# Kernel tuning notes

Hardware: AMD Instinct MI355X
Metric: run time of the kernel (lower is better)

Reference implementation:

```python
import jax, jax.numpy as jnp
import numpy as np

V, D_IMG, D_H = 10000, 768, 512
B, N, T = 16, 196, 128
LN_EPS = 1e-5

def _lin_w(k, fan_out, fan_in):
    bound = 1.0 / np.sqrt(fan_in)
    return jax.random.uniform(k, (fan_out, fan_in), jnp.float32, -bound, bound)

def _lin_b(k, fan_out, fan_in):
    bound = 1.0 / np.sqrt(fan_in)
    return jax.random.uniform(k, (fan_out,), jnp.float32, -bound, bound)

def setup_inputs() -> dict:
    key = jax.random.key(0)
    ks = jax.random.split(key, 24)
    patches = jax.random.normal(ks[0], (B, N, D_IMG), jnp.float32)
    cls = jax.random.normal(ks[1], (B, D_IMG), jnp.float32)
    tgt_ids = jax.random.randint(ks[2], (B, T), 0, V)
    emb = jax.random.normal(ks[3], (V, D_H), jnp.float32)
    emb = emb.at[0].set(0.0)  # padding_idx=0
    inp = {
        "patches": patches, "cls": cls, "tgt_ids": tgt_ids,
        "kv_w": _lin_w(ks[4], D_H, D_IMG), "kv_b": _lin_b(ks[5], D_H, D_IMG),
        "ih_w": _lin_w(ks[6], D_H, D_IMG), "ih_b": _lin_b(ks[7], D_H, D_IMG),
        "ic_w": _lin_w(ks[8], D_H, D_IMG), "ic_b": _lin_b(ks[9], D_H, D_IMG),
        "emb": emb,
        "attn_Wh": _lin_w(ks[10], D_H, D_H),
        "attn_Wk": _lin_w(ks[11], D_H, D_H),
        "attn_v": _lin_w(ks[12], 1, D_H),
        "lstm_Wih": _lin_w(ks[13], 4 * D_H, D_H),  # pytorch init uses 1/sqrt(hidden)
        "lstm_Whh": _lin_w(ks[14], 4 * D_H, D_H),
        "lstm_bih": _lin_b(ks[15], 4 * D_H, D_H),
        "lstm_bhh": _lin_b(ks[16], 4 * D_H, D_H),
        "ln_g": jnp.ones((D_H,), jnp.float32),
        "ln_b": jnp.zeros((D_H,), jnp.float32),
        "out_w": _lin_w(ks[17], V, D_H), "out_b": _lin_b(ks[18], V, D_H),
    }
    # lstm_Wih actually has fan_in 2*D_H but torch inits with 1/sqrt(hidden_size); reshape to correct shape
    inp["lstm_Wih"] = _lin_w(ks[19], 4 * D_H, 2 * D_H)
    return inp

def _layernorm(x, g, b):
    mu = jnp.mean(x, -1, keepdims=True)
    var = jnp.mean(jnp.square(x - mu), -1, keepdims=True)
    return (x - mu) * jax.lax.rsqrt(var + LN_EPS) * g + b

def reference(patches, cls, tgt_ids, kv_w, kv_b, ih_w, ih_b, ic_w, ic_b, emb,
              attn_Wh, attn_Wk, attn_v, lstm_Wih, lstm_Whh, lstm_bih, lstm_bhh,
              ln_g, ln_b, out_w, out_b):
    keys = patches @ kv_w.T + kv_b            # (B,N,d_h)
    keysWk = keys @ attn_Wk.T                 # precompute W_k(keys), loop-invariant
    h0 = cls @ ih_w.T + ih_b                  # (B,d_h)
    c0 = cls @ ic_w.T + ic_b
    x_all = emb[tgt_ids]                      # (B,T,d_h)
    vvec = attn_v[0]                          # (d_h,)

    def step(carry, x_t):
        h, c = carry
        energy = jnp.tanh((h @ attn_Wh.T)[:, None, :] + keysWk)   # (B,N,d_h)
        scores = energy @ vvec                                    # (B,N)
        alpha = jax.nn.softmax(scores, axis=-1)
        ctx = jnp.einsum('bn,bnd->bd', alpha, keys)               # (B,d_h)
        z = jnp.concatenate([x_t, ctx], axis=-1)                  # (B,2*d_h)
        gates = z @ lstm_Wih.T + lstm_bih + h @ lstm_Whh.T + lstm_bhh
        i, f, g, o = jnp.split(gates, 4, axis=-1)
        c_new = jax.nn.sigmoid(f) * c + jax.nn.sigmoid(i) * jnp.tanh(g)
        h_raw = jax.nn.sigmoid(o) * jnp.tanh(c_new)
        h_new = _layernorm(h_raw, ln_g, ln_b)  # dropout is identity in eval
        logits_t = h_new @ out_w.T + out_b     # (B,V)
        return (h_new, c_new), logits_t

    (_, _), logits = jax.lax.scan(step, (h0, c0), jnp.swapaxes(x_all, 0, 1))
    return jnp.swapaxes(logits, 0, 1)          # (B,T,V)
```

## Files before the change

### kernel.cpp

```cpp
#include <hip/hip_runtime.h>
#include <hip/hip_bf16.h>

#define T_STEPS 128
#define DH      512
#define NPATCH  196
#define BATCH   16
#define VOCAB   10000
#define NB5     64

typedef __attribute__((ext_vector_type(8))) short bf16x8;
typedef __attribute__((ext_vector_type(4))) float f32x4;

__device__ __forceinline__ float sigm(float x) { return 1.0f / (1.0f + __expf(-x)); }
__device__ __forceinline__ float ftanh(float x) {
    float e = __expf(2.0f * x);
    return 1.0f - 2.0f / (e + 1.0f);
}
__device__ __forceinline__ unsigned short f2b(float x) {
    union { float f; unsigned u; } v; v.f = x;
    unsigned r = (v.u + 0x7FFFu + ((v.u >> 16) & 1u)) >> 16;
    return (unsigned short)r;
}
__device__ __forceinline__ float b2f(unsigned short h) {
    union { unsigned u; float f; } v; v.u = ((unsigned)h) << 16;
    return v.f;
}
__device__ __forceinline__ float cload(const float* p) {
    return __hip_atomic_load(p, __ATOMIC_RELAXED, __HIP_MEMORY_SCOPE_AGENT);
}
__device__ __forceinline__ void cstore(float* p, float v) {
    __hip_atomic_store(p, v, __ATOMIC_RELAXED, __HIP_MEMORY_SCOPE_AGENT);
}
__device__ __forceinline__ f32x4 cload4(const float* p) {
    f32x4 v;
    asm volatile("global_load_dwordx4 %0, %1, off sc0 sc1\n\ts_waitcnt vmcnt(0)"
                 : "=&v"(v) : "v"(p) : "memory");
    return v;
}
__device__ __forceinline__ void cload4x2(const float* p0, const float* p1, f32x4& a, f32x4& b) {
    asm volatile("global_load_dwordx4 %0, %2, off sc0 sc1\n\t"
                 "global_load_dwordx4 %1, %3, off sc0 sc1\n\t"
                 "s_waitcnt vmcnt(0)"
                 : "=&v"(a), "=&v"(b) : "v"(p0), "v"(p1) : "memory");
}
__device__ __forceinline__ void cstore4(float* p, f32x4 v) {
    asm volatile("global_store_dwordx4 %0, %1, off sc0 sc1" :: "v"(p), "v"(v) : "memory");
}

__global__ __launch_bounds__(256)
void cvt_kernel(const float* __restrict__ src, unsigned short* __restrict__ dst, int n)
{
    int i = (blockIdx.x * 256 + threadIdx.x) * 8;
    if (i >= n) return;
    float4 v0 = *(const float4*)(src + i);
    float4 v1 = *(const float4*)(src + i + 4);
    float xs[8] = {v0.x, v0.y, v0.z, v0.w, v1.x, v1.y, v1.z, v1.w};
    bf16x8 o;
#pragma unroll
    for (int j = 0; j < 8; ++j) o[j] = (short)f2b(xs[j]);
    *(bf16x8*)(dst + i) = o;
}

__global__ __launch_bounds__(256)
void cvt_split_kernel(const float* __restrict__ src, unsigned short* __restrict__ hi,
                      unsigned short* __restrict__ lo, int n)
{
    int i = (blockIdx.x * 256 + threadIdx.x) * 8;
    if (i >= n) return;
    float4 v0 = *(const float4*)(src + i);
    float4 v1 = *(const float4*)(src + i + 4);
    float xs[8] = {v0.x, v0.y, v0.z, v0.w, v1.x, v1.y, v1.z, v1.w};
    bf16x8 h_, l_;
#pragma unroll
    for (int j = 0; j < 8; ++j) {
        unsigned short hb = f2b(xs[j]);
        float r = xs[j] - b2f(hb);
        h_[j] = (short)hb;
        l_[j] = (short)f2b(r);
    }
    *(bf16x8*)(hi + i) = h_;
    *(bf16x8*)(lo + i) = l_;
}

__global__ __launch_bounds__(256)
void cvt_wx_kernel(const float* __restrict__ Wih, unsigned short* __restrict__ WxH,
                   unsigned short* __restrict__ WxL)
{
    int i = (blockIdx.x * 256 + threadIdx.x) * 8;
    if (i >= 2048 * 512) return;
    int j = i >> 9, k = i & 511;
    const float* s = Wih + (size_t)j * 1024 + k;
    float4 v0 = *(const float4*)s, v1 = *(const float4*)(s + 4);
    float xs[8] = {v0.x, v0.y, v0.z, v0.w, v1.x, v1.y, v1.z, v1.w};
    bf16x8 h_, l_;
#pragma unroll
    for (int q = 0; q < 8; ++q) {
        unsigned short hb = f2b(xs[q]);
        h_[q] = (short)hb;
        l_[q] = (short)f2b(xs[q] - b2f(hb));
    }
    *(bf16x8*)(WxH + i) = h_;
    *(bf16x8*)(WxL + i) = l_;
}

__global__ __launch_bounds__(256)
void gemm_mfma(const unsigned short* __restrict__ AH, const unsigned short* __restrict__ AL,
               const unsigned short* __restrict__ WH, const unsigned short* __restrict__ WL,
               const float* __restrict__ bias, float* __restrict__ C,
               unsigned short* __restrict__ CbH, unsigned short* __restrict__ CbL,
               int M, int N, int K)
{
    const int tid = threadIdx.x, wid = tid >> 6, l = tid & 63;
    const int m0 = blockIdx.x * 128 + (wid >> 1) * 64;
    const int n0 = blockIdx.y * 128 + (wid & 1) * 64;
    const int lm = l & 15, lk = (l >> 4) * 8;
    f32x4 acc[4][4];
#pragma unroll
    for (int i = 0; i < 4; ++i)
#pragma unroll
        for (int j = 0; j < 4; ++j) acc[i][j] = (f32x4){0.f, 0.f, 0.f, 0.f};
    const bf16x8 az = {0,0,0,0,0,0,0,0};

    for (int k0 = 0; k0 < K; k0 += 32) {
        bf16x8 aH[4], aL[4];
#pragma unroll
        for (int mi = 0; mi < 4; ++mi) {
            int m = m0 + mi * 16 + lm;
            aH[mi] = (m < M) ? *(const bf16x8*)(AH + (size_t)m * K + k0 + lk) : az;
            aL[mi] = (AL && m < M) ? *(const bf16x8*)(AL + (size_t)m * K + k0 + lk) : az;
        }
#pragma unroll
        for (int ni = 0; ni < 4; ++ni) {
            int n = n0 + ni * 16 + lm;
            bf16x8 bH = az, bL = az;
            if (n < N) {
                bH = *(const bf16x8*)(WH + (size_t)n * K + k0 + lk);
                if (WL) bL = *(const bf16x8*)(WL + (size_t)n * K + k0 + lk);
            }
#pragma unroll
            for (int mi = 0; mi < 4; ++mi) {
                acc[mi][ni] = __builtin_amdgcn_mfma_f32_16x16x32_bf16(aH[mi], bH, acc[mi][ni], 0, 0, 0);
                if (WL) acc[mi][ni] = __builtin_amdgcn_mfma_f32_16x16x32_bf16(aH[mi], bL, acc[mi][ni], 0, 0, 0);
                if (AL) acc[mi][ni] = __builtin_amdgcn_mfma_f32_16x16x32_bf16(aL[mi], bH, acc[mi][ni], 0, 0, 0);
            }
        }
    }
    const int rr = (l >> 4) * 4;
#pragma unroll
    for (int mi = 0; mi < 4; ++mi) {
        int mb = m0 + mi * 16 + rr;
#pragma unroll
        for (int ni = 0; ni < 4; ++ni) {
            int n = n0 + ni * 16 + lm;
            if (n < N) {
                float bs = bias ? bias[n] : 0.f;
#pragma unroll
                for (int r = 0; r < 4; ++r) {
                    int mm = mb + r;
                    if (mm < M) {
                        float v = acc[mi][ni][r] + bs;
                        if (C)   C[(size_t)mm * N + n] = v;
                        if (CbH) {
                            unsigned short hb = f2b(v);
                            CbH[(size_t)mm * N + n] = hb;
                            if (CbL) CbL[(size_t)mm * N + n] = f2b(v - b2f(hb));
                        }
                    }
                }
            }
        }
    }
}

__global__ __launch_bounds__(256)
void h0c0_kernel(const float* __restrict__ cls,
                 const float* __restrict__ ihw, const float* __restrict__ ihb,
                 const float* __restrict__ icw, const float* __restrict__ icb,
                 float* __restrict__ c_g, float* __restrict__ h_raw0)
{
    int id = blockIdx.x * 256 + threadIdx.x;
    int which = id >> 13;
    int b = (id >> 9) & 15;
    int d = id & 511;
    const float* w = (which ? icw : ihw) + d * 768;
    const float* x = cls + b * 768;
    float acc = which ? icb[d] : ihb[d];
    const float4* x4 = (const float4*)x;
    const float4* w4 = (const float4*)w;
#pragma unroll 4
    for (int k = 0; k < 192; ++k) {
        float4 a = x4[k], ww = w4[k];
        acc += a.x * ww.x + a.y * ww.y + a.z * ww.z + a.w * ww.w;
    }
    if (which) c_g[b * 512 + d] = acc;
    else h_raw0[b * 512 + d] = acc;
}

__global__ __launch_bounds__(256)
void gather_kernel(const int* __restrict__ ids, const float* __restrict__ emb,
                   unsigned short* __restrict__ xH, unsigned short* __restrict__ xL)
{
    int q = blockIdx.x * 256 + threadIdx.x;
    if (q >= 2048 * 64) return;
    int r = q >> 6, c = (q & 63) * 8;
    int tgt = ids[r];
    const float4* s = (const float4*)(emb + (size_t)tgt * 512 + c);
    float4 v0 = s[0], v1 = s[1];
    float xs[8] = {v0.x, v0.y, v0.z, v0.w, v1.x, v1.y, v1.z, v1.w};
    bf16x8 oh, ol;
#pragma unroll
    for (int j = 0; j < 8; ++j) {
        unsigned short hb = f2b(xs[j]);
        oh[j] = (short)hb;
        ol[j] = (short)f2b(xs[j] - b2f(hb));
    }
    *(bf16x8*)(xH + (size_t)r * 512 + c) = oh;
    *(bf16x8*)(xL + (size_t)r * 512 + c) = ol;
}

__device__ __forceinline__ void grid_bar(int* slots, int gen)
{
    __syncthreads();
    if (threadIdx.x < 64) {
        if (threadIdx.x == 0)
            __hip_atomic_store(&slots[blockIdx.x], gen, __ATOMIC_RELAXED, __HIP_MEMORY_SCOPE_AGENT);
        while (__hip_atomic_load(&slots[threadIdx.x], __ATOMIC_RELAXED, __HIP_MEMORY_SCOPE_AGENT) < gen)
            __builtin_amdgcn_s_sleep(1);
    }
    __syncthreads();
}
__device__ __forceinline__ void group_bar(int* gslots, int b_own, int q, int gen)
{
    __syncthreads();
    if (threadIdx.x < 4) {
        if (threadIdx.x == 0)
            __hip_atomic_store(&gslots[b_own * 4 + q], gen, __ATOMIC_RELAXED, __HIP_MEMORY_SCOPE_AGENT);
        while (__hip_atomic_load(&gslots[b_own * 4 + threadIdx.x], __ATOMIC_RELAXED, __HIP_MEMORY_SCOPE_AGENT) < gen)
            __builtin_amdgcn_s_sleep(1);
    }
    __syncthreads();
}

__global__ __launch_bounds__(1024, 2)
void recur6_kernel(float* __restrict__ ctx, float* __restrict__ hln_g,
                   float* __restrict__ h_raw2, float* __restrict__ c_g,
                   float* __restrict__ partials2, float* __restrict__ ew_g,
                   float* __restrict__ sc_g,
                   const float* __restrict__ keys, const float* __restrict__ keysWk,
                   const float* __restrict__ XG,
                   const float* __restrict__ Wih, const float* __restrict__ Whh,
                   const float* __restrict__ bih, const float* __restrict__ bhh,
                   const float* __restrict__ Wh, const float* __restrict__ lng,
                   const float* __restrict__ lnb, const float* __restrict__ vvec,
                   unsigned short* __restrict__ h_all_b, int* __restrict__ bar)
{
    __shared__ float zs[8][1024];
    __shared__ float hv[512], ewS[512], vvS[512];
    __shared__ float alS[200];
    __shared__ float pb[8][128];
    __shared__ float gbuf[16][32];
    __shared__ float bias_l[32], red[32];

    const int k = blockIdx.x, tid = threadIdx.x;
    const int b_own = k & 15, q = k >> 4;
    const int rrow = tid >> 5, ks = tid & 31;
    int* gslots = bar + 64;

    float wreg[32];
    {
        int g = rrow >> 3, dd = rrow & 7;
        int j = g * 512 + 8 * k + dd;
        const float* wc = Wih + (size_t)j * 1024 + 512;
        const float* wh2 = Whh + (size_t)j * 512;
#pragma unroll
        for (int i = 0; i < 32; ++i) {
            int kk = ks + 32 * i;
            wreg[i] = (kk < 512) ? wc[kk] : wh2[kk - 512];
        }
        if (tid < 32) {
            int g2 = tid >> 3, dd2 = tid & 7, j2 = g2 * 512 + 8 * k + dd2;
            bias_l[tid] = bih[j2] + bhh[j2];
        }
        if (tid < 512) vvS[tid] = vvec[tid];
    }
    __syncthreads();

    int gen = 0;
    for (int t = 0; t < T_STEPS; ++t) {
        const float* hcur = h_raw2 + (t & 1) * (BATCH * 512);
        float* hnxt = h_raw2 + ((t + 1) & 1) * (BATCH * 512);
        const float* pcur = partials2 + (t & 1) * (BATCH * 64 * 2);
        float* pnxt = partials2 + ((t + 1) & 1) * (BATCH * 64 * 2);

        if (t > 0) {
            if (tid < 64) {
                const float* pp = pcur + ((size_t)b_own * 64 + tid) * 2;
                float s1 = cload(pp), s2 = cload(pp + 1);
#pragma unroll
                for (int m = 1; m < 64; m <<= 1) { s1 += __shfl_xor(s1, m); s2 += __shfl_xor(s2, m); }
                if (tid == 0) {
                    float mu = s1 * (1.f / 512.f);
                    float var = s2 * (1.f / 512.f) - mu * mu;
                    red[0] = mu; red[1] = rsqrtf(var + 1e-5f);
                }
            }
        } else if (tid == 0) { red[0] = 0.f; red[1] = 1.f; }
        __syncthreads();
        if (tid < 128) {
            f32x4 h4 = cload4(hcur + b_own * 512 + tid * 4);
            f32x4 o = h4;
            if (t > 0) {
                float mu = red[0], rv = red[1];
                f32x4 g4 = ((const f32x4*)lng)[tid];
                f32x4 bl4 = ((const f32x4*)lnb)[tid];
#pragma unroll
                for (int u = 0; u < 4; ++u) o[u] = (h4[u] - mu) * rv * g4[u] + bl4[u];
            }
            ((f32x4*)hv)[tid] = o;
            if (q == 0) {
                cstore4(&hln_g[b_own * 512 + tid * 4], o);
                if (t > 0) {
                    short4 hb = { (short)f2b(o[0]), (short)f2b(o[1]), (short)f2b(o[2]), (short)f2b(o[3]) };
                    *(short4*)(h_all_b + ((size_t)b_own * T_STEPS + (t - 1)) * 512 + tid * 4) = hb;
                }
            }
        }
        __syncthreads();
        {
            int e = q * 128 + (tid >> 3), g8 = tid & 7;
            const float4* wr4 = (const float4*)(Wh + (size_t)e * 512);
            float s = 0.f;
#pragma unroll
            for (int i = 0; i < 16; ++i) {
                int k4 = g8 + 8 * i;
                float4 w4 = wr4[k4];
                float4 h4 = ((const float4*)hv)[k4];
                s += w4.x * h4.x + w4.y * h4.y + w4.z * h4.z + w4.w * h4.w;
            }
            s += __shfl_xor(s, 1); s += __shfl_xor(s, 2); s += __shfl_xor(s, 4);
            if (g8 == 0) cstore(&ew_g[b_own * 512 + e], s);
        }
        group_bar(gslots, b_own, q, ++gen);

        if (tid < 128) ((f32x4*)ewS)[tid] = cload4(&ew_g[b_own * 512 + tid * 4]);
        __syncthreads();
        {
            int nl = tid >> 4, s16 = tid & 15;
            if (nl < 49) {
                int n = q * 49 + nl;
                const float4* kw4 = (const float4*)(keysWk + ((size_t)(b_own * NPATCH + n)) * 512);
                float s = 0.f;
#pragma unroll
                for (int i = 0; i < 8; ++i) {
                    int k4 = s16 + 16 * i;
                    float4 kk = kw4[k4];
                    int d0 = k4 * 4;
                    s += ftanh(ewS[d0 + 0] + kk.x) * vvS[d0 + 0]
                       + ftanh(ewS[d0 + 1] + kk.y) * vvS[d0 + 1]
                       + ftanh(ewS[d0 + 2] + kk.z) * vvS[d0 + 2]
                       + ftanh(ewS[d0 + 3] + kk.w) * vvS[d0 + 3];
                }
                s += __shfl_xor(s, 1); s += __shfl_xor(s, 2);
                s += __shfl_xor(s, 4); s += __shfl_xor(s, 8);
                if (s16 == 0) cstore(&sc_g[b_own * NPATCH + n], s);
            }
        }
        group_bar(gslots, b_own, q, ++gen);

        {
            float sv = (tid < NPATCH) ? cload(&sc_g[b_own * NPATCH + tid]) : -1e30f;
            float m1 = sv;
#pragma unroll
            for (int m = 1; m < 64; m <<= 1) m1 = fmaxf(m1, __shfl_xor(m1, m));
            if ((tid & 63) == 0 && tid < 256) red[8 + (tid >> 6)] = m1;
            __syncthreads();
            float mx = fmaxf(fmaxf(red[8], red[9]), fmaxf(red[10], red[11]));
            float ev = (tid < NPATCH) ? __expf(sv - mx) : 0.f;
            if (tid < NPATCH) alS[tid] = ev;
            float s2 = ev;
#pragma unroll
            for (int m = 1; m < 64; m <<= 1) s2 += __shfl_xor(s2, m);
            if ((tid & 63) == 0 && tid < 256) red[12 + (tid >> 6)] = s2;
            __syncthreads();
            float inv = 1.f / (red[12] + red[13] + red[14] + red[15]);
            int d_loc = tid & 127, g8 = tid >> 7;
            const float* kb = keys + (size_t)(b_own * NPATCH) * 512 + q * 128 + d_loc;
            float acc = 0.f;
            for (int n = g8; n < NPATCH; n += 8) acc += alS[n] * kb[(size_t)n * 512];
            pb[g8][d_loc] = acc;
            __syncthreads();
            if (tid < 128) {
                float s = 0.f;
#pragma unroll
                for (int g = 0; g < 8; ++g) s += pb[g][tid];
                cstore(&ctx[b_own * 512 + q * 128 + tid], s * inv);
            }
        }
        grid_bar(bar, ++gen);

#pragma unroll
        for (int p = 0; p < 2; ++p) {
            {
                int bb = tid >> 7, i4 = (tid & 127) * 4;
                int b = p * 8 + bb;
                f32x4 c4, h4;
                cload4x2(&ctx[b * 512 + i4], &hln_g[b * 512 + i4], c4, h4);
                *(f32x4*)&zs[bb][i4] = c4;
                *(f32x4*)&zs[bb][512 + i4] = h4;
            }
            __syncthreads();
#pragma unroll
            for (int bl = 0; bl < 8; ++bl) {
                float acc = 0.f;
#pragma unroll
                for (int i = 0; i < 32; ++i) acc += wreg[i] * zs[bl][ks + 32 * i];
#pragma unroll
                for (int m = 1; m < 32; m <<= 1) acc += __shfl_xor(acc, m);
                if (ks == 0) gbuf[p * 8 + bl][rrow] = acc;
            }
            __syncthreads();
        }
        if (tid < 128) {
            int bp = tid >> 3, dd = tid & 7, d = 8 * k + dd;
            const float* xg = XG + ((size_t)bp * T_STEPS + t) * 2048;
            float gi = gbuf[bp][dd]      + bias_l[dd]      + xg[d];
            float gf = gbuf[bp][8 + dd]  + bias_l[8 + dd]  + xg[512 + d];
            float gg = gbuf[bp][16 + dd] + bias_l[16 + dd] + xg[1024 + d];
            float go = gbuf[bp][24 + dd] + bias_l[24 + dd] + xg[1536 + d];
            float cn = sigm(gf) * c_g[bp * 512 + d] + sigm(gi) * ftanh(gg);
            c_g[bp * 512 + d] = cn;
            float hr = sigm(go) * ftanh(cn);
            cstore(&hnxt[bp * 512 + d], hr);
            float s1 = hr, s2 = hr * hr;
#pragma unroll
            for (int m = 1; m < 8; m <<= 1) { s1 += __shfl_xor(s1, m); s2 += __shfl_xor(s2, m); }
            if (dd == 0) {
                cstore(&pnxt[((size_t)bp * 64 + k) * 2 + 0], s1);
                cstore(&pnxt[((size_t)bp * 64 + k) * 2 + 1], s2);
            }
        }
        grid_bar(bar, ++gen);
    }

    if (q == 0) {
        const float* hcur = h_raw2 + (T_STEPS & 1) * (BATCH * 512);
        const float* pcur = partials2 + (T_STEPS & 1) * (BATCH * 64 * 2);
        int b = b_own;
        if (tid < 64) {
            const float* pp = pcur + ((size_t)b * 64 + tid) * 2;
            float s1 = cload(pp), s2 = cload(pp + 1);
#pragma unroll
            for (int m = 1; m < 64; m <<= 1) { s1 += __shfl_xor(s1, m); s2 += __shfl_xor(s2, m); }
            if (tid == 0) {
                float mu = s1 * (1.f / 512.f);
                float var = s2 * (1.f / 512.f) - mu * mu;
                red[0] = mu; red[1] = rsqrtf(var + 1e-5f);
            }
        }
        __syncthreads();
        if (tid < 128) {
            f32x4 h4 = cload4(hcur + b * 512 + tid * 4);
            float mu = red[0], rv = red[1];
            f32x4 g4 = ((const f32x4*)lng)[tid];
            f32x4 bl4 = ((const f32x4*)lnb)[tid];
            f32x4 o;
#pragma unroll
            for (int u = 0; u < 4; ++u) o[u] = (h4[u] - mu) * rv * g4[u] + bl4[u];
            short4 hb = { (short)f2b(o[0]), (short)f2b(o[1]), (short)f2b(o[2]), (short)f2b(o[3]) };
            *(short4*)(h_all_b + ((size_t)b * T_STEPS + (T_STEPS - 1)) * 512 + tid * 4) = hb;
        }
    }
}

extern "C" void kernel_launch(void* const* d_in, const int* in_sizes, int n_in,
                              void* d_out, int out_size, void* d_ws, size_t ws_size,
                              hipStream_t stream)
{
    const float* patches = (const float*)d_in[0];
    const float* cls     = (const float*)d_in[1];
    const int*   tgt     = (const int*)d_in[2];
    const float* kv_w    = (const float*)d_in[3];
    const float* kv_b    = (const float*)d_in[4];
    const float* ih_w    = (const float*)d_in[5];
    const float* ih_b    = (const float*)d_in[6];
    const float* ic_w    = (const float*)d_in[7];
    const float* ic_b    = (const float*)d_in[8];
    const float* emb     = (const float*)d_in[9];
    const float* Wh      = (const float*)d_in[10];
    const float* Wk      = (const float*)d_in[11];
    const float* av      = (const float*)d_in[12];
    const float* Wih     = (const float*)d_in[13];
    const float* Whh     = (const float*)d_in[14];
    const float* bih     = (const float*)d_in[15];
    const float* bhh     = (const float*)d_in[16];
    const float* lng     = (const float*)d_in[17];
    const float* lnb     = (const float*)d_in[18];
    const float* outw    = (const float*)d_in[19];
    const float* outb    = (const float*)d_in[20];
    float* out = (float*)d_out;

    char* wsp = (char*)d_ws;
    auto carve = [&](size_t bytes) -> char* {
        char* p = wsp; wsp += (bytes + 255) & ~(size_t)255; return p;
    };
    float*          keys_f   = (float*)carve((size_t)3136 * 512 * 4);
    float*          keysWk_f = (float*)carve((size_t)3136 * 512 * 4);
    unsigned short* keysH    = (unsigned short*)carve((size_t)3136 * 512 * 2);
    unsigned short* keysL    = (unsigned short*)carve((size_t)3136 * 512 * 2);
    unsigned short* xH       = (unsigned short*)carve((size_t)2048 * 512 * 2);
    unsigned short* xL       = (unsigned short*)carve((size_t)2048 * 512 * 2);
    unsigned short* h_all_b  = (unsigned short*)carve((size_t)2048 * 512 * 2);
    unsigned short* wxH      = (unsigned short*)carve((size_t)2048 * 512 * 2);
    unsigned short* wxL      = (unsigned short*)carve((size_t)2048 * 512 * 2);
    unsigned short* kvwH     = (unsigned short*)carve((size_t)512 * 768 * 2);
    unsigned short* kvwL     = (unsigned short*)carve((size_t)512 * 768 * 2);
    unsigned short* wkH      = (unsigned short*)carve((size_t)512 * 512 * 2);
    unsigned short* wkL      = (unsigned short*)carve((size_t)512 * 512 * 2);
    char*           R1       = carve((size_t)2048 * 2048 * 4);
    float* ctx      = (float*)carve((size_t)16 * 512 * 4);
    float* hln_g    = (float*)carve((size_t)16 * 512 * 4);
    float* h_raw2   = (float*)carve((size_t)2 * 16 * 512 * 4);
    float* c_g      = (float*)carve((size_t)16 * 512 * 4);
    float* partials2= (float*)carve((size_t)2 * 16 * 64 * 2 * 4);
    float* ew_g     = (float*)carve((size_t)16 * 512 * 4);
    float* sc_g     = (float*)carve((size_t)16 * NPATCH * 4);
    int*   bar      = (int*)carve(8192);
    unsigned short* patH   = (unsigned short*)R1;
    unsigned short* patL   = (unsigned short*)R1 + (size_t)3136 * 768;
    float*          XG     = (float*)R1;
    unsigned short* outw_b = (unsigned short*)R1;

    (void)hipMemsetAsync(bar, 0, 8192, stream);

    auto cvt = [&](const float* s, unsigned short* d, int n) {
        cvt_kernel<<<(n / 8 + 255) / 256, 256, 0, stream>>>(s, d, n);
    };
    auto cvts = [&](const float* s, unsigned short* dh, unsigned short* dl, int n) {
        cvt_split_kernel<<<(n / 8 + 255) / 256, 256, 0, stream>>>(s, dh, dl, n);
    };
    cvts(patches, patH, patL, 3136 * 768);
    cvts(kv_w, kvwH, kvwL, 512 * 768);
    cvts(Wk, wkH, wkL, 512 * 512);
    cvt_wx_kernel<<<512, 256, 0, stream>>>(Wih, wxH, wxL);
    gather_kernel<<<512, 256, 0, stream>>>(tgt, emb, xH, xL);

    gemm_mfma<<<dim3(25, 4), 256, 0, stream>>>(patH, patL, kvwH, kvwL, kv_b,
                                               keys_f, keysH, keysL, 3136, 512, 768);
    gemm_mfma<<<dim3(25, 4), 256, 0, stream>>>(keysH, keysL, wkH, wkL, nullptr,
                                               keysWk_f, nullptr, nullptr, 3136, 512, 512);
    gemm_mfma<<<dim3(16, 16), 256, 0, stream>>>(xH, xL, wxH, wxL, nullptr,
                                                XG, nullptr, nullptr, 2048, 2048, 512);

    h0c0_kernel<<<64, 256, 0, stream>>>(cls, ih_w, ih_b, ic_w, ic_b, c_g, h_raw2);

    recur6_kernel<<<NB5, 1024, 0, stream>>>(ctx, hln_g, h_raw2, c_g, partials2, ew_g, sc_g,
                                            keys_f, keysWk_f, XG, Wih, Whh, bih, bhh, Wh,
                                            lng, lnb, av, h_all_b, bar);

    cvt(outw, outw_b, VOCAB * 512);
    gemm_mfma<<<dim3(16, 79), 256, 0, stream>>>(h_all_b, nullptr, outw_b, nullptr, outb,
                                                out, nullptr, nullptr, 2048, VOCAB, 512);
}
```

Baseline: 5.004 ms.

## Compute attention energy and scores redundantly per block to drop group barriers

Each of the four blocks sharing a batch row now computes the full W_h·h projection and all 196 attention scores itself in shared memory. Before, the four blocks split that work, exchanged results through global memory and met at two cross-block group barriers per step. The gate matvec also stages all 16 batch rows at once in a larger shared buffer instead of two passes of 8. The cost is four times the redundant work on those two stages and more shared memory per block, with the launch-bounds occupancy hint lowered from 2 blocks to 1.

Result: slower. 6.571 ms (+31.3%).

```diff
diff --git a/kernel.cpp b/kernel.cpp
--- a/kernel.cpp
+++ b/kernel.cpp
@@ -229,23 +229,11 @@
     }
     __syncthreads();
 }
-__device__ __forceinline__ void group_bar(int* gslots, int b_own, int q, int gen)
-{
-    __syncthreads();
-    if (threadIdx.x < 4) {
-        if (threadIdx.x == 0)
-            __hip_atomic_store(&gslots[b_own * 4 + q], gen, __ATOMIC_RELAXED, __HIP_MEMORY_SCOPE_AGENT);
-        while (__hip_atomic_load(&gslots[b_own * 4 + threadIdx.x], __ATOMIC_RELAXED, __HIP_MEMORY_SCOPE_AGENT) < gen)
-            __builtin_amdgcn_s_sleep(1);
-    }
-    __syncthreads();
-}
-
-__global__ __launch_bounds__(1024, 2)
-void recur6_kernel(float* __restrict__ ctx, float* __restrict__ hln_g,
+
+__global__ __launch_bounds__(1024, 1)
+void recur7_kernel(float* __restrict__ ctx, float* __restrict__ hln_g,
                    float* __restrict__ h_raw2, float* __restrict__ c_g,
-                   float* __restrict__ partials2, float* __restrict__ ew_g,
-                   float* __restrict__ sc_g,
+                   float* __restrict__ partials2,
                    const float* __restrict__ keys, const float* __restrict__ keysWk,
                    const float* __restrict__ XG,
                    const float* __restrict__ Wih, const float* __restrict__ Whh,
@@ -254,9 +242,9 @@
                    const float* __restrict__ lnb, const float* __restrict__ vvec,
                    unsigned short* __restrict__ h_all_b, int* __restrict__ bar)
 {
-    __shared__ float zs[8][1024];
+    __shared__ float zs[16][1024];
     __shared__ float hv[512], ewS[512], vvS[512];
-    __shared__ float alS[200];
+    __shared__ float scS[200], alS[200];
     __shared__ float pb[8][128];
     __shared__ float gbuf[16][32];
     __shared__ float bias_l[32], red[32];
@@ -264,7 +252,6 @@
     const int k = blockIdx.x, tid = threadIdx.x;
     const int b_own = k & 15, q = k >> 4;
     const int rrow = tid >> 5, ks = tid & 31;
-    int* gslots = bar + 64;
 
     float wreg[32];
     {
@@ -327,48 +314,50 @@
         }
         __syncthreads();
         {
-            int e = q * 128 + (tid >> 3), g8 = tid & 7;
-            const float4* wr4 = (const float4*)(Wh + (size_t)e * 512);
-            float s = 0.f;
-#pragma unroll
-            for (int i = 0; i < 16; ++i) {
-                int k4 = g8 + 8 * i;
-                float4 w4 = wr4[k4];
-                float4 h4 = ((const float4*)hv)[k4];
-                s += w4.x * h4.x + w4.y * h4.y + w4.z * h4.z + w4.w * h4.w;
-            }
-            s += __shfl_xor(s, 1); s += __shfl_xor(s, 2); s += __shfl_xor(s, 4);
-            if (g8 == 0) cstore(&ew_g[b_own * 512 + e], s);
-        }
-        group_bar(gslots, b_own, q, ++gen);
-
-        if (tid < 128) ((f32x4*)ewS)[tid] = cload4(&ew_g[b_own * 512 + tid * 4]);
+            int g8 = tid & 7;
+#pragma unroll
+            for (int pass = 0; pass < 4; ++pass) {
+                int e = pass * 128 + (tid >> 3);
+                const float4* wr4 = (const float4*)(Wh + (size_t)e * 512);
+                float s = 0.f;
+#pragma unroll
+                for (int i = 0; i < 16; ++i) {
+                    int k4 = g8 + 8 * i;
+                    float4 w4 = wr4[k4];
+                    float4 h4 = ((const float4*)hv)[k4];
+                    s += w4.x * h4.x + w4.y * h4.y + w4.z * h4.z + w4.w * h4.w;
+                }
+                s += __shfl_xor(s, 1); s += __shfl_xor(s, 2); s += __shfl_xor(s, 4);
+                if (g8 == 0) ewS[e] = s;
+            }
+        }
         __syncthreads();
         {
-            int nl = tid >> 4, s16 = tid & 15;
-            if (nl < 49) {
-                int n = q * 49 + nl;
-                const float4* kw4 = (const float4*)(keysWk + ((size_t)(b_own * NPATCH + n)) * 512);
-                float s = 0.f;
-#pragma unroll
-                for (int i = 0; i < 8; ++i) {
-                    int k4 = s16 + 16 * i;
-                    float4 kk = kw4[k4];
-                    int d0 = k4 * 4;
-                    s += ftanh(ewS[d0 + 0] + kk.x) * vvS[d0 + 0]
-                       + ftanh(ewS[d0 + 1] + kk.y) * vvS[d0 + 1]
-                       + ftanh(ewS[d0 + 2] + kk.z) * vvS[d0 + 2]
-                       + ftanh(ewS[d0 + 3] + kk.w) * vvS[d0 + 3];
+            int g8 = tid & 7;
+#pragma unroll
+            for (int pass = 0; pass < 2; ++pass) {
+                int n = pass * 128 + (tid >> 3);
+                if (n < NPATCH) {
+                    const float4* kw4 = (const float4*)(keysWk + ((size_t)(b_own * NPATCH + n)) * 512);
+                    float s = 0.f;
+#pragma unroll
+                    for (int i = 0; i < 16; ++i) {
+                        int k4 = g8 + 8 * i;
+                        float4 kk = kw4[k4];
+                        int d0 = k4 * 4;
+                        s += ftanh(ewS[d0 + 0] + kk.x) * vvS[d0 + 0]
+                           + ftanh(ewS[d0 + 1] + kk.y) * vvS[d0 + 1]
+                           + ftanh(ewS[d0 + 2] + kk.z) * vvS[d0 + 2]
+                           + ftanh(ewS[d0 + 3] + kk.w) * vvS[d0 + 3];
+                    }
+                    s += __shfl_xor(s, 1); s += __shfl_xor(s, 2); s += __shfl_xor(s, 4);
+                    if (g8 == 0) scS[n] = s;
                 }
-                s += __shfl_xor(s, 1); s += __shfl_xor(s, 2);
-                s += __shfl_xor(s, 4); s += __shfl_xor(s, 8);
-                if (s16 == 0) cstore(&sc_g[b_own * NPATCH + n], s);
-            }
-        }
-        group_bar(gslots, b_own, q, ++gen);
-
+            }
+        }
+        __syncthreads();
         {
-            float sv = (tid < NPATCH) ? cload(&sc_g[b_own * NPATCH + tid]) : -1e30f;
+            float sv = (tid < NPATCH) ? scS[tid] : -1e30f;
             float m1 = sv;
 #pragma unroll
             for (int m = 1; m < 64; m <<= 1) m1 = fmaxf(m1, __shfl_xor(m1, m));
@@ -398,28 +387,26 @@
         }
         grid_bar(bar, ++gen);
 
-#pragma unroll
-        for (int p = 0; p < 2; ++p) {
-            {
-                int bb = tid >> 7, i4 = (tid & 127) * 4;
-                int b = p * 8 + bb;
-                f32x4 c4, h4;
-                cload4x2(&ctx[b * 512 + i4], &hln_g[b * 512 + i4], c4, h4);
-                *(f32x4*)&zs[bb][i4] = c4;
-                *(f32x4*)&zs[bb][512 + i4] = h4;
-            }
-            __syncthreads();
-#pragma unroll
-            for (int bl = 0; bl < 8; ++bl) {
-                float acc = 0.f;
-#pragma unroll
-                for (int i = 0; i < 32; ++i) acc += wreg[i] * zs[bl][ks + 32 * i];
-#pragma unroll
-                for (int m = 1; m < 32; m <<= 1) acc += __shfl_xor(acc, m);
-                if (ks == 0) gbuf[p * 8 + bl][rrow] = acc;
-            }
-            __syncthreads();
-        }
+        {
+            int bb = tid >> 6, off = (tid & 63) * 16;
+            const float* src = (off < 512) ? &ctx[bb * 512 + off] : &hln_g[bb * 512 + (off - 512)];
+            f32x4 a0, a1, a2, a3;
+            cload4x2(src, src + 4, a0, a1);
+            cload4x2(src + 8, src + 12, a2, a3);
+            f32x4* dst = (f32x4*)&zs[bb][off];
+            dst[0] = a0; dst[1] = a1; dst[2] = a2; dst[3] = a3;
+        }
+        __syncthreads();
+#pragma unroll
+        for (int bl = 0; bl < 16; ++bl) {
+            float acc = 0.f;
+#pragma unroll
+            for (int i = 0; i < 32; ++i) acc += wreg[i] * zs[bl][ks + 32 * i];
+#pragma unroll
+            for (int m = 1; m < 32; m <<= 1) acc += __shfl_xor(acc, m);
+            if (ks == 0) gbuf[bl][rrow] = acc;
+        }
+        __syncthreads();
         if (tid < 128) {
             int bp = tid >> 3, dd = tid & 7, d = 8 * k + dd;
             const float* xg = XG + ((size_t)bp * T_STEPS + t) * 2048;
@@ -522,8 +509,6 @@
     float* h_raw2   = (float*)carve((size_t)2 * 16 * 512 * 4);
     float* c_g      = (float*)carve((size_t)16 * 512 * 4);
     float* partials2= (float*)carve((size_t)2 * 16 * 64 * 2 * 4);
-    float* ew_g     = (float*)carve((size_t)16 * 512 * 4);
-    float* sc_g     = (float*)carve((size_t)16 * NPATCH * 4);
     int*   bar      = (int*)carve(8192);
     unsigned short* patH   = (unsigned short*)R1;
     unsigned short* patL   = (unsigned short*)R1 + (size_t)3136 * 768;
@@ -553,7 +538,7 @@
 
     h0c0_kernel<<<64, 256, 0, stream>>>(cls, ih_w, ih_b, ic_w, ic_b, c_g, h_raw2);
 
-    recur6_kernel<<<NB5, 1024, 0, stream>>>(ctx, hln_g, h_raw2, c_g, partials2, ew_g, sc_g,
+    recur7_kernel<<<NB5, 1024, 0, stream>>>(ctx, hln_g, h_raw2, c_g, partials2,
                                             keys_f, keysWk_f, XG, Wih, Whh, bih, bhh, Wh,
                                             lng, lnb, av, h_all_b, bar);
 
```
